# Optimization experiments

Measured on AMD Instinct MI355X. Metric: run time of the kernel, lower is better.

## Reference

```python
import jax, jax.numpy as jnp
import numpy as np

# --- hashgrid config (from __init__: num_levels=16, level_dim=4, base_res=2, log2_hashmap_size=19, desired_res=2048) ---
NUM_LEVELS = 16
LEVEL_DIM = 4
BASE_RES = 2
DESIRED_RES = 2048
TABLE_SIZE = 2 ** 19
_b = np.exp((np.log(DESIRED_RES) - np.log(BASE_RES)) / (NUM_LEVELS - 1))
SCALES = BASE_RES * _b ** np.arange(NUM_LEVELS) - 1.0          # instant-ngp per-level scale
RES = (np.ceil(SCALES) + 1).astype(np.int64)                   # per-level grid resolution
PRIME = np.uint32(2654435761)                                  # 2D spatial hash prime


def softplus10(x):
    return jax.nn.softplus(10.0 * x) / 10.0


def hash_encode(u, tables):
    """u: [P,2] in [0,1]; tables: [L, TABLE_SIZE, LEVEL_DIM]. Returns [P, L*LEVEL_DIM]."""
    outs = []
    for l in range(NUM_LEVELS):
        s = float(SCALES[l])
        res = int(RES[l])
        pos = u * s + 0.5
        pf = jnp.floor(pos)
        fr = pos - pf                      # bilinear fractions, [P,2]
        pi = pf.astype(jnp.int32)
        acc = None
        for dx in (0, 1):
            for dy in (0, 1):
                cx = pi[:, 0] + dx
                cy = pi[:, 1] + dy
                if res * res <= TABLE_SIZE:
                    idx = cy * res + cx                                   # dense level
                else:
                    idx = (cx.astype(jnp.uint32) ^ (cy.astype(jnp.uint32) * PRIME)) % jnp.uint32(TABLE_SIZE)
                    idx = idx.astype(jnp.int32)                           # hashed level
                wx = fr[:, 0] if dx else 1.0 - fr[:, 0]
                wy = fr[:, 1] if dy else 1.0 - fr[:, 1]
                term = tables[l][idx] * (wx * wy)[:, None]                # gather + bilerp
                acc = term if acc is None else acc + term
        outs.append(acc)
    return jnp.concatenate(outs, axis=-1)


def setup_inputs() -> dict:
    key = jax.random.key(0)
    ks = jax.random.split(key, 4)
    B, N, T = 4, 2048, 192
    x = jax.random.normal(ks[0], (B, N, T, 2), jnp.float32)
    embeddings = jax.random.normal(ks[1], (NUM_LEVELS, TABLE_SIZE, LEVEL_DIM), jnp.float32) * 1e-2
    W0 = jax.random.normal(ks[2], (64, 64), jnp.float32) / 8.0
    b0 = jnp.zeros((64,), jnp.float32)
    W1 = jax.random.normal(ks[3], (64, 1), jnp.float32) / 8.0
    b1 = jnp.zeros((1,), jnp.float32)
    return {"x": x, "embeddings": embeddings, "W0": W0, "b0": b0, "W1": W1, "b1": b1}


def reference(x, embeddings, W0, b0, W1, b1):
    B, N, T = x.shape[:3]
    xf = x.reshape(-1, T, 2)                       # [B*N, T, 2]
    rays_o = xf[:, 0]
    rd = xf[:, -1] - xf[:, 0]
    rd = rd / jnp.linalg.norm(rd, axis=-1, keepdims=True)
    z = jnp.linspace(0.0, 2.0, T)                  # [T]
    sample_dist = 1.0 / T
    xys = rays_o[:, None, :] + rd[:, None, :] * z[None, :, None]   # [B*N, T, 2]
    xys = jnp.clip(xys, -1.0, 1.0)                 # aabb clamp [-1,-1,1,1]
    u = (xys.reshape(-1, 2) + 1.0) * 0.5           # map [-bound,bound] -> [0,1], bound=1
    feats = hash_encode(u, embeddings)             # [P, 64]
    h = softplus10(feats @ W0 + b0)
    sigma = softplus10(h @ W1 + b1).reshape(-1, T) # [B*N, T]
    deltas = jnp.concatenate([jnp.full((1,), sample_dist, sigma.dtype), z[1:] - z[:-1]])  # [T]
    density = (deltas[None, :] * sigma).reshape(B, N, T)
    return density
```

## Files before the change

### kernel.cpp

```cpp
#include <hip/hip_runtime.h>
#include <cmath>
#include <algorithm>

#define NUM_LEVELS 16
#define TABLE_SIZE 524288
#define TMASK (TABLE_SIZE - 1)
#define HASH_PRIME 2654435761u
#define T_SAMPLES 192
#define BLOCK 256
#define PTS 64
#define CHUNK 4096

typedef __bf16 bf16x8 __attribute__((ext_vector_type(8)));
typedef __bf16 bf16x4 __attribute__((ext_vector_type(4)));
typedef float f32x4 __attribute__((ext_vector_type(4)));
typedef short s16x4 __attribute__((ext_vector_type(4)));

struct LvlParams {
    float s[NUM_LEVELS];
    int   res[NUM_LEVELS];
    int   hashed[NUM_LEVELS];
    int   off[NUM_LEVELS];
    int   used[NUM_LEVELS];
};

__device__ __forceinline__ float softplus10(float x) {
    float t = 10.0f * x;
    float e = __expf(-fabsf(t));
    return (fmaxf(t, 0.0f) + __logf(1.0f + e)) * 0.1f;
}

__device__ __forceinline__ void corner_idx(int cx, int cy, int res, int hashed,
                                           int& i00, int& i01, int& i10, int& i11) {
    if (hashed) {
        unsigned hy0 = (unsigned)cy * HASH_PRIME;
        unsigned hy1 = (unsigned)(cy + 1) * HASH_PRIME;
        i00 = (int)(((unsigned)cx ^ hy0) & TMASK);
        i01 = (int)(((unsigned)cx ^ hy1) & TMASK);
        i10 = (int)(((unsigned)(cx + 1) ^ hy0) & TMASK);
        i11 = (int)(((unsigned)(cx + 1) ^ hy1) & TMASK);
    } else {
        i00 = cy * res + cx; i10 = i00 + 1;
        i01 = i00 + res;     i11 = i01 + 1;
    }
}

__device__ __forceinline__ bf16x4 lerp4(f32x4 c00, f32x4 c01, f32x4 c10, f32x4 c11,
                                        float fx, float fy) {
    float w00 = (1.0f - fx) * (1.0f - fy), w01 = (1.0f - fx) * fy;
    float w10 = fx * (1.0f - fy),          w11 = fx * fy;
    f32x4 a = c00 * w00 + c01 * w01 + c10 * w10 + c11 * w11;
    bf16x4 r;
    r[0] = (__bf16)a.x; r[1] = (__bf16)a.y; r[2] = (__bf16)a.z; r[3] = (__bf16)a.w;
    return r;
}

__global__ void prep(const float* __restrict__ W0, __bf16* __restrict__ w0f,
                     float* __restrict__ sArr, int* __restrict__ resArr,
                     int* __restrict__ hashArr, int* __restrict__ offArr,
                     int* __restrict__ usedArr, LvlParams lp) {
    const int t = threadIdx.x;
    if (t < NUM_LEVELS) {
        sArr[t] = lp.s[t]; resArr[t] = lp.res[t]; hashArr[t] = lp.hashed[t];
        offArr[t] = lp.off[t]; usedArr[t] = lp.used[t];
    }
    #pragma unroll
    for (int i = 0; i < 16; ++i) {
        int f = t * 16 + i;
        int j = f & 7, lx = (f >> 3) & 15, q = (f >> 7) & 3, nt = (f >> 9) & 3, kc = f >> 11;
        int k = kc * 32 + q * 8 + j;
        int n = nt * 16 + lx;
        w0f[f] = (__bf16)W0[k * 64 + n];
    }
}

__global__ void prep_tables(const float* __restrict__ emb, short* __restrict__ embq,
                            float* __restrict__ scaleArr,
                            const int* __restrict__ offArr, const int* __restrict__ usedArr) {
    __shared__ float red[256];
    const int l    = blockIdx.y;
    const int used = usedArr[l];
    const int base = blockIdx.x * CHUNK;
    if (base >= used) return;
    const int t = threadIdx.x;
    const float* src = emb + ((size_t)l * TABLE_SIZE + base) * 4;

    f32x4 v[16];
    float m = 0.0f;
    #pragma unroll
    for (int i = 0; i < 16; ++i) {
        int e = t + 256 * i;
        if (base + e < used) {
            v[i] = *(const f32x4*)(src + (size_t)e * 4);
            m = fmaxf(m, fmaxf(fmaxf(fabsf(v[i].x), fabsf(v[i].y)),
                               fmaxf(fabsf(v[i].z), fabsf(v[i].w))));
        } else v[i] = (f32x4)(0.0f);
    }
    red[t] = m;
    __syncthreads();
    for (int s = 128; s > 0; s >>= 1) {
        if (t < s) red[t] = fmaxf(red[t], red[t + s]);
        __syncthreads();
    }
    const float mx  = red[0];
    const float inv = (mx > 0.0f) ? (32767.0f / mx) : 0.0f;
    const int chunkIdx = (offArr[l] >> 12) + blockIdx.x;
    if (t == 0) scaleArr[chunkIdx] = (mx > 0.0f) ? (mx / 32767.0f) : 0.0f;

    short* dst = embq + (size_t)(offArr[l] + base) * 4;
    #pragma unroll
    for (int i = 0; i < 16; ++i) {
        int e = t + 256 * i;
        if (base + e < used) {
            s16x4 q;
            q[0] = (short)__float2int_rn(v[i].x * inv);
            q[1] = (short)__float2int_rn(v[i].y * inv);
            q[2] = (short)__float2int_rn(v[i].z * inv);
            q[3] = (short)__float2int_rn(v[i].w * inv);
            *(s16x4*)(dst + (size_t)e * 4) = q;
        }
    }
}

template<bool QT>
__launch_bounds__(BLOCK, 8)
__global__ void nerf_fused(const float* __restrict__ x,
                           const float* __restrict__ emb,
                           const short* __restrict__ embq,
                           const float* __restrict__ scaleArr,
                           const __bf16* __restrict__ w0f,
                           const float* __restrict__ sArr,
                           const int* __restrict__ resArr,
                           const int* __restrict__ hashArr,
                           const int* __restrict__ offArr,
                           const float* __restrict__ b0,
                           const float* __restrict__ W1,
                           const float* __restrict__ b1,
                           float* __restrict__ out) {
    __shared__ __align__(16) __bf16 feT[NUM_LEVELS * PTS * 4];

    const int tid  = threadIdx.x;
    const int lane = tid & 63, w = tid >> 6;

    const int gp  = blockIdx.x * PTS + lane;
    const int ray = gp / T_SAMPLES;
    const int t   = gp - ray * T_SAMPLES;

    const float2 o  = *(const float2*)(x + (size_t)ray * (T_SAMPLES * 2));
    const float2 ep = *(const float2*)(x + (size_t)ray * (T_SAMPLES * 2) + (T_SAMPLES - 1) * 2);
    float rdx = ep.x - o.x, rdy = ep.y - o.y;
    float inv = 1.0f / sqrtf(rdx * rdx + rdy * rdy);
    rdx *= inv; rdy *= inv;
    const float z = (float)((double)t * (2.0 / 191.0));
    float px = fminf(fmaxf(o.x + rdx * z, -1.0f), 1.0f);
    float py = fminf(fmaxf(o.y + rdy * z, -1.0f), 1.0f);
    const float ux = (px + 1.0f) * 0.5f;
    const float uy = (py + 1.0f) * 0.5f;

    const int l3 = w + 12;

    f32x4 c3v[4]; float fx3, fy3;
    {
        float s = sArr[l3];
        float posx = ux * s + 0.5f, posy = uy * s + 0.5f;
        float pfx = floorf(posx), pfy = floorf(posy);
        fx3 = posx - pfx; fy3 = posy - pfy;
        int cx = (int)pfx, cy = (int)pfy;
        int i00, i01, i10, i11;
        corner_idx(cx, cy, resArr[l3], hashArr[l3], i00, i01, i10, i11);
        if (QT) {
            const s16x4* tb = (const s16x4*)embq + offArr[l3];
            const int cb = offArr[l3] >> 12;
            s16x4 r0 = tb[i00], r1 = tb[i01], r2 = tb[i10], r3 = tb[i11];
            c3v[0] = __builtin_convertvector(r0, f32x4) * scaleArr[cb + (i00 >> 12)];
            c3v[1] = __builtin_convertvector(r1, f32x4) * scaleArr[cb + (i01 >> 12)];
            c3v[2] = __builtin_convertvector(r2, f32x4) * scaleArr[cb + (i10 >> 12)];
            c3v[3] = __builtin_convertvector(r3, f32x4) * scaleArr[cb + (i11 >> 12)];
        } else {
            const f32x4* tb = (const f32x4*)(emb + (size_t)l3 * (TABLE_SIZE * 4));
            c3v[0] = tb[i00]; c3v[1] = tb[i01]; c3v[2] = tb[i10]; c3v[3] = tb[i11];
        }
    }

    #pragma unroll
    for (int li = 0; li < 3; ++li) {
        const int l = w + li * 4;
        float s = sArr[l];
        float posx = ux * s + 0.5f, posy = uy * s + 0.5f;
        float pfx = floorf(posx), pfy = floorf(posy);
        float fx = posx - pfx, fy = posy - pfy;
        int cx = (int)pfx, cy = (int)pfy;
        int res = resArr[l];
        int i00 = cy * res + cx, i10 = i00 + 1, i01 = i00 + res, i11 = i01 + 1;
        f32x4 a, b, c, d;
        if (QT) {
            const s16x4* tb = (const s16x4*)embq + offArr[l];
            const int cb = offArr[l] >> 12;
            s16x4 r0 = tb[i00], r1 = tb[i01], r2 = tb[i10], r3 = tb[i11];
            a = __builtin_convertvector(r0, f32x4) * scaleArr[cb + (i00 >> 12)];
            b = __builtin_convertvector(r1, f32x4) * scaleArr[cb + (i01 >> 12)];
            c = __builtin_convertvector(r2, f32x4) * scaleArr[cb + (i10 >> 12)];
            d = __builtin_convertvector(r3, f32x4) * scaleArr[cb + (i11 >> 12)];
        } else {
            const f32x4* tb = (const f32x4*)(emb + (size_t)l * (TABLE_SIZE * 4));
            a = tb[i00]; b = tb[i01]; c = tb[i10]; d = tb[i11];
        }
        *(bf16x4*)&feT[(l * PTS + lane) * 4] = lerp4(a, b, c, d, fx, fy);
    }

    *(bf16x4*)&feT[(l3 * PTS + lane) * 4] = lerp4(c3v[0], c3v[1], c3v[2], c3v[3], fx3, fy3);

    __syncthreads();

    const int lx = lane & 15, q = lane >> 4;
    const int p  = w * 16 + lx;

    f32x4 acc[4];
    #pragma unroll
    for (int nt = 0; nt < 4; ++nt) acc[nt] = (f32x4)(0.0f);

    #pragma unroll
    for (int kc = 0; kc < 2; ++kc) {
        const int la = kc * 8 + 2 * q;
        bf16x4 lo = *(const bf16x4*)&feT[(la * PTS + p) * 4];
        bf16x4 hi = *(const bf16x4*)&feT[((la + 1) * PTS + p) * 4];
        bf16x8 afr = __builtin_shufflevector(lo, hi, 0, 1, 2, 3, 4, 5, 6, 7);
        #pragma unroll
        for (int nt = 0; nt < 4; ++nt) {
            bf16x8 bfr = *(const bf16x8*)(w0f + (size_t)(((kc * 4 + nt) * 4 + q) * 16 + lx) * 8);
            acc[nt] = __builtin_amdgcn_mfma_f32_16x16x32_bf16(afr, bfr, acc[nt], 0, 0, 0);
        }
    }

    float b0v[4], w1v[4];
    #pragma unroll
    for (int nt = 0; nt < 4; ++nt) {
        b0v[nt] = b0[nt * 16 + lx];
        w1v[nt] = W1[nt * 16 + lx];
    }
    const float b1v = b1[0];
    const float d0 = (float)(1.0 / 192.0);
    const float d1 = (float)(2.0 / 191.0);

    float part[4];
    #pragma unroll
    for (int r = 0; r < 4; ++r) {
        float pp = 0.0f;
        #pragma unroll
        for (int nt = 0; nt < 4; ++nt)
            pp += softplus10(acc[nt][r] + b0v[nt]) * w1v[nt];
        pp += __shfl_xor(pp, 1, 64);
        pp += __shfl_xor(pp, 2, 64);
        pp += __shfl_xor(pp, 4, 64);
        pp += __shfl_xor(pp, 8, 64);
        part[r] = pp;
    }
    if (lx == 0) {
        const int g0 = blockIdx.x * PTS + w * 16 + q * 4;
        const int tt = g0 % T_SAMPLES;
        f32x4 ov;
        ov.x = softplus10(part[0] + b1v) * (tt == 0 ? d0 : d1);
        ov.y = softplus10(part[1] + b1v) * d1;
        ov.z = softplus10(part[2] + b1v) * d1;
        ov.w = softplus10(part[3] + b1v) * d1;
        *(f32x4*)(out + g0) = ov;
    }
}

extern "C" void kernel_launch(void* const* d_in, const int* in_sizes, int n_in,
                              void* d_out, int out_size, void* d_ws, size_t ws_size,
                              hipStream_t stream) {
    const float* x   = (const float*)d_in[0];
    const float* emb = (const float*)d_in[1];
    const float* W0  = (const float*)d_in[2];
    const float* b0  = (const float*)d_in[3];
    const float* W1  = (const float*)d_in[4];
    const float* b1  = (const float*)d_in[5];
    float* out = (float*)d_out;

    char* ws = (char*)d_ws;
    __bf16* w0f    = (__bf16*)ws;
    float*  sArr   = (float*)(ws + 8192);
    int*    resArr = (int*)(ws + 8256);
    int*    hashArr= (int*)(ws + 8320);
    int*    offArr = (int*)(ws + 8384);
    int*    usedArr= (int*)(ws + 8448);
    float*  scaleArr = (float*)(ws + 8704);
    short*  embq   = (short*)(ws + 16384);

    LvlParams lp;
    const double bb = std::exp((std::log(2048.0) - std::log(2.0)) / 15.0);
    int off = 0, maxUsed = 0;
    for (int l = 0; l < NUM_LEVELS; ++l) {
        double sc = 2.0 * std::pow(bb, (double)l) - 1.0;
        int rr = (int)std::ceil(sc) + 1;
        lp.s[l] = (float)sc;
        lp.res[l] = rr;
        lp.hashed[l] = ((long long)rr * (long long)rr > (long long)TABLE_SIZE) ? 1 : 0;
        int used;
        if (lp.hashed[l]) {
            used = TABLE_SIZE;
        } else {
            long long cmax = (long long)std::floor(sc + 0.5) + 1;
            long long u = cmax * (long long)rr + cmax + 1 + (rr + 2);
            used = (int)std::min((long long)TABLE_SIZE, u);
        }
        lp.off[l]  = off;
        lp.used[l] = used;
        off += (used + CHUNK - 1) & ~(CHUNK - 1);
        if (used > maxUsed) maxUsed = used;
    }
    const size_t need = 16384 + (size_t)off * 4 * sizeof(short);
    const bool useQ = ws_size >= need;

    prep<<<1, 256, 0, stream>>>(W0, w0f, sArr, resArr, hashArr, offArr, usedArr, lp);

    const int nblk = out_size / PTS;
    if (useQ) {
        dim3 pg((maxUsed + CHUNK - 1) / CHUNK, NUM_LEVELS);
        prep_tables<<<pg, 256, 0, stream>>>(emb, embq, scaleArr, offArr, usedArr);
        nerf_fused<true><<<nblk, BLOCK, 0, stream>>>(x, emb, embq, scaleArr, w0f,
                                                     sArr, resArr, hashArr, offArr,
                                                     b0, W1, b1, out);
    } else {
        nerf_fused<false><<<nblk, BLOCK, 0, stream>>>(x, emb, embq, scaleArr, w0f,
                                                      sArr, resArr, hashArr, offArr,
                                                      b0, W1, b1, out);
    }
}
```

Measured before the change: 356.1 us.

## Store hash tables in fp16, drop per-chunk scales, and switch MFMA to f16

Replaces the int16 per-chunk-scaled table quantization with a plain fp16 table copy, which removes the max-reduction in the prep kernel and the scale lookups on every gather. Bilinear interpolation now runs in packed fp16, and the MLP's first layer uses the f16 MFMA instead of bf16. The softplus constants are folded into the bias and W1 scaling, and the hash recomputes hy1 by adding the prime instead of multiplying. fp16 has less dynamic range than the scaled int16 format, and doing the interpolation in half precision adds rounding error.

```diff
diff --git a/kernel.cpp b/kernel.cpp
--- a/kernel.cpp
+++ b/kernel.cpp
@@ -11,10 +11,11 @@
 #define PTS 64
 #define CHUNK 4096
 
-typedef __bf16 bf16x8 __attribute__((ext_vector_type(8)));
-typedef __bf16 bf16x4 __attribute__((ext_vector_type(4)));
+typedef _Float16 f16;
+typedef f16 f16x2 __attribute__((ext_vector_type(2)));
+typedef f16 f16x4 __attribute__((ext_vector_type(4)));
+typedef f16 f16x8 __attribute__((ext_vector_type(8)));
 typedef float f32x4 __attribute__((ext_vector_type(4)));
-typedef short s16x4 __attribute__((ext_vector_type(4)));
 
 struct LvlParams {
     float s[NUM_LEVELS];
@@ -34,7 +35,7 @@
                                            int& i00, int& i01, int& i10, int& i11) {
     if (hashed) {
         unsigned hy0 = (unsigned)cy * HASH_PRIME;
-        unsigned hy1 = (unsigned)(cy + 1) * HASH_PRIME;
+        unsigned hy1 = hy0 + HASH_PRIME;
         i00 = (int)(((unsigned)cx ^ hy0) & TMASK);
         i01 = (int)(((unsigned)cx ^ hy1) & TMASK);
         i10 = (int)(((unsigned)(cx + 1) ^ hy0) & TMASK);
@@ -45,17 +46,25 @@
     }
 }
 
-__device__ __forceinline__ bf16x4 lerp4(f32x4 c00, f32x4 c01, f32x4 c10, f32x4 c11,
+__device__ __forceinline__ f16x4 lerp4h(f16x4 c00, f16x4 c01, f16x4 c10, f16x4 c11,
+                                        float fx, float fy) {
+    float gx = 1.0f - fx, gy = 1.0f - fy;
+    f16 w00 = (f16)(gx * gy), w01 = (f16)(gx * fy);
+    f16 w10 = (f16)(fx * gy), w11 = (f16)(fx * fy);
+    f16x4 v00 = {w00, w00, w00, w00}, v01 = {w01, w01, w01, w01};
+    f16x4 v10 = {w10, w10, w10, w10}, v11 = {w11, w11, w11, w11};
+    return c00 * v00 + c01 * v01 + c10 * v10 + c11 * v11;
+}
+
+__device__ __forceinline__ f16x4 lerp4f(f32x4 c00, f32x4 c01, f32x4 c10, f32x4 c11,
                                         float fx, float fy) {
     float w00 = (1.0f - fx) * (1.0f - fy), w01 = (1.0f - fx) * fy;
     float w10 = fx * (1.0f - fy),          w11 = fx * fy;
     f32x4 a = c00 * w00 + c01 * w01 + c10 * w10 + c11 * w11;
-    bf16x4 r;
-    r[0] = (__bf16)a.x; r[1] = (__bf16)a.y; r[2] = (__bf16)a.z; r[3] = (__bf16)a.w;
-    return r;
-}
-
-__global__ void prep(const float* __restrict__ W0, __bf16* __restrict__ w0f,
+    return __builtin_convertvector(a, f16x4);
+}
+
+__global__ void prep(const float* __restrict__ W0, f16* __restrict__ w0f,
                      float* __restrict__ sArr, int* __restrict__ resArr,
                      int* __restrict__ hashArr, int* __restrict__ offArr,
                      int* __restrict__ usedArr, LvlParams lp) {
@@ -70,54 +79,25 @@
         int j = f & 7, lx = (f >> 3) & 15, q = (f >> 7) & 3, nt = (f >> 9) & 3, kc = f >> 11;
         int k = kc * 32 + q * 8 + j;
         int n = nt * 16 + lx;
-        w0f[f] = (__bf16)W0[k * 64 + n];
-    }
-}
-
-__global__ void prep_tables(const float* __restrict__ emb, short* __restrict__ embq,
-                            float* __restrict__ scaleArr,
+        w0f[f] = (f16)W0[k * 64 + n];
+    }
+}
+
+__global__ void prep_tables(const float* __restrict__ emb, f16* __restrict__ embq,
                             const int* __restrict__ offArr, const int* __restrict__ usedArr) {
-    __shared__ float red[256];
     const int l    = blockIdx.y;
     const int used = usedArr[l];
     const int base = blockIdx.x * CHUNK;
     if (base >= used) return;
     const int t = threadIdx.x;
     const float* src = emb + ((size_t)l * TABLE_SIZE + base) * 4;
-
-    f32x4 v[16];
-    float m = 0.0f;
+    f16* dst = embq + (size_t)(offArr[l] + base) * 4;
     #pragma unroll
     for (int i = 0; i < 16; ++i) {
         int e = t + 256 * i;
         if (base + e < used) {
-            v[i] = *(const f32x4*)(src + (size_t)e * 4);
-            m = fmaxf(m, fmaxf(fmaxf(fabsf(v[i].x), fabsf(v[i].y)),
-                               fmaxf(fabsf(v[i].z), fabsf(v[i].w))));
-        } else v[i] = (f32x4)(0.0f);
-    }
-    red[t] = m;
-    __syncthreads();
-    for (int s = 128; s > 0; s >>= 1) {
-        if (t < s) red[t] = fmaxf(red[t], red[t + s]);
-        __syncthreads();
-    }
-    const float mx  = red[0];
-    const float inv = (mx > 0.0f) ? (32767.0f / mx) : 0.0f;
-    const int chunkIdx = (offArr[l] >> 12) + blockIdx.x;
-    if (t == 0) scaleArr[chunkIdx] = (mx > 0.0f) ? (mx / 32767.0f) : 0.0f;
-
-    short* dst = embq + (size_t)(offArr[l] + base) * 4;
-    #pragma unroll
-    for (int i = 0; i < 16; ++i) {
-        int e = t + 256 * i;
-        if (base + e < used) {
-            s16x4 q;
-            q[0] = (short)__float2int_rn(v[i].x * inv);
-            q[1] = (short)__float2int_rn(v[i].y * inv);
-            q[2] = (short)__float2int_rn(v[i].z * inv);
-            q[3] = (short)__float2int_rn(v[i].w * inv);
-            *(s16x4*)(dst + (size_t)e * 4) = q;
+            f32x4 v = *(const f32x4*)(src + (size_t)e * 4);
+            *(f16x4*)(dst + (size_t)e * 4) = __builtin_convertvector(v, f16x4);
         }
     }
 }
@@ -126,9 +106,8 @@
 __launch_bounds__(BLOCK, 8)
 __global__ void nerf_fused(const float* __restrict__ x,
                            const float* __restrict__ emb,
-                           const short* __restrict__ embq,
-                           const float* __restrict__ scaleArr,
-                           const __bf16* __restrict__ w0f,
+                           const f16* __restrict__ embq,
+                           const f16* __restrict__ w0f,
                            const float* __restrict__ sArr,
                            const int* __restrict__ resArr,
                            const int* __restrict__ hashArr,
@@ -137,7 +116,7 @@
                            const float* __restrict__ W1,
                            const float* __restrict__ b1,
                            float* __restrict__ out) {
-    __shared__ __align__(16) __bf16 feT[NUM_LEVELS * PTS * 4];
+    __shared__ __align__(16) f16 feT[NUM_LEVELS * PTS * 4];
 
     const int tid  = threadIdx.x;
     const int lane = tid & 63, w = tid >> 6;
@@ -159,7 +138,7 @@
 
     const int l3 = w + 12;
 
-    f32x4 c3v[4]; float fx3, fy3;
+    f16x4 c3v[4]; float fx3, fy3;
     {
         float s = sArr[l3];
         float posx = ux * s + 0.5f, posy = uy * s + 0.5f;
@@ -169,16 +148,15 @@
         int i00, i01, i10, i11;
         corner_idx(cx, cy, resArr[l3], hashArr[l3], i00, i01, i10, i11);
         if (QT) {
-            const s16x4* tb = (const s16x4*)embq + offArr[l3];
-            const int cb = offArr[l3] >> 12;
-            s16x4 r0 = tb[i00], r1 = tb[i01], r2 = tb[i10], r3 = tb[i11];
-            c3v[0] = __builtin_convertvector(r0, f32x4) * scaleArr[cb + (i00 >> 12)];
-            c3v[1] = __builtin_convertvector(r1, f32x4) * scaleArr[cb + (i01 >> 12)];
-            c3v[2] = __builtin_convertvector(r2, f32x4) * scaleArr[cb + (i10 >> 12)];
-            c3v[3] = __builtin_convertvector(r3, f32x4) * scaleArr[cb + (i11 >> 12)];
+            const f16x4* tb = (const f16x4*)embq + offArr[l3];
+            c3v[0] = tb[i00]; c3v[1] = tb[i01]; c3v[2] = tb[i10]; c3v[3] = tb[i11];
         } else {
             const f32x4* tb = (const f32x4*)(emb + (size_t)l3 * (TABLE_SIZE * 4));
-            c3v[0] = tb[i00]; c3v[1] = tb[i01]; c3v[2] = tb[i10]; c3v[3] = tb[i11];
+            f32x4 a = tb[i00], b = tb[i01], c = tb[i10], d = tb[i11];
+            c3v[0] = __builtin_convertvector(a, f16x4);
+            c3v[1] = __builtin_convertvector(b, f16x4);
+            c3v[2] = __builtin_convertvector(c, f16x4);
+            c3v[3] = __builtin_convertvector(d, f16x4);
         }
     }
 
@@ -192,23 +170,18 @@
         int cx = (int)pfx, cy = (int)pfy;
         int res = resArr[l];
         int i00 = cy * res + cx, i10 = i00 + 1, i01 = i00 + res, i11 = i01 + 1;
-        f32x4 a, b, c, d;
         if (QT) {
-            const s16x4* tb = (const s16x4*)embq + offArr[l];
-            const int cb = offArr[l] >> 12;
-            s16x4 r0 = tb[i00], r1 = tb[i01], r2 = tb[i10], r3 = tb[i11];
-            a = __builtin_convertvector(r0, f32x4) * scaleArr[cb + (i00 >> 12)];
-            b = __builtin_convertvector(r1, f32x4) * scaleArr[cb + (i01 >> 12)];
-            c = __builtin_convertvector(r2, f32x4) * scaleArr[cb + (i10 >> 12)];
-            d = __builtin_convertvector(r3, f32x4) * scaleArr[cb + (i11 >> 12)];
+            const f16x4* tb = (const f16x4*)embq + offArr[l];
+            f16x4 a = tb[i00], b = tb[i01], c = tb[i10], d = tb[i11];
+            *(f16x4*)&feT[(l * PTS + lane) * 4] = lerp4h(a, b, c, d, fx, fy);
         } else {
             const f32x4* tb = (const f32x4*)(emb + (size_t)l * (TABLE_SIZE * 4));
-            a = tb[i00]; b = tb[i01]; c = tb[i10]; d = tb[i11];
-        }
-        *(bf16x4*)&feT[(l * PTS + lane) * 4] = lerp4(a, b, c, d, fx, fy);
-    }
-
-    *(bf16x4*)&feT[(l3 * PTS + lane) * 4] = lerp4(c3v[0], c3v[1], c3v[2], c3v[3], fx3, fy3);
+            f32x4 a = tb[i00], b = tb[i01], c = tb[i10], d = tb[i11];
+            *(f16x4*)&feT[(l * PTS + lane) * 4] = lerp4f(a, b, c, d, fx, fy);
+        }
+    }
+
+    *(f16x4*)&feT[(l3 * PTS + lane) * 4] = lerp4h(c3v[0], c3v[1], c3v[2], c3v[3], fx3, fy3);
 
     __syncthreads();
 
@@ -222,21 +195,21 @@
     #pragma unroll
     for (int kc = 0; kc < 2; ++kc) {
         const int la = kc * 8 + 2 * q;
-        bf16x4 lo = *(const bf16x4*)&feT[(la * PTS + p) * 4];
-        bf16x4 hi = *(const bf16x4*)&feT[((la + 1) * PTS + p) * 4];
-        bf16x8 afr = __builtin_shufflevector(lo, hi, 0, 1, 2, 3, 4, 5, 6, 7);
+        f16x4 lo = *(const f16x4*)&feT[(la * PTS + p) * 4];
+        f16x4 hi = *(const f16x4*)&feT[((la + 1) * PTS + p) * 4];
+        f16x8 afr = __builtin_shufflevector(lo, hi, 0, 1, 2, 3, 4, 5, 6, 7);
         #pragma unroll
         for (int nt = 0; nt < 4; ++nt) {
-            bf16x8 bfr = *(const bf16x8*)(w0f + (size_t)(((kc * 4 + nt) * 4 + q) * 16 + lx) * 8);
-            acc[nt] = __builtin_amdgcn_mfma_f32_16x16x32_bf16(afr, bfr, acc[nt], 0, 0, 0);
-        }
-    }
-
-    float b0v[4], w1v[4];
+            f16x8 bfr = *(const f16x8*)(w0f + (size_t)(((kc * 4 + nt) * 4 + q) * 16 + lx) * 8);
+            acc[nt] = __builtin_amdgcn_mfma_f32_16x16x32_f16(afr, bfr, acc[nt], 0, 0, 0);
+        }
+    }
+
+    float b010[4], w1s[4];
     #pragma unroll
     for (int nt = 0; nt < 4; ++nt) {
-        b0v[nt] = b0[nt * 16 + lx];
-        w1v[nt] = W1[nt * 16 + lx];
+        b010[nt] = b0[nt * 16 + lx] * 10.0f;
+        w1s[nt]  = W1[nt * 16 + lx] * 0.1f;
     }
     const float b1v = b1[0];
     const float d0 = (float)(1.0 / 192.0);
@@ -247,8 +220,12 @@
     for (int r = 0; r < 4; ++r) {
         float pp = 0.0f;
         #pragma unroll
-        for (int nt = 0; nt < 4; ++nt)
-            pp += softplus10(acc[nt][r] + b0v[nt]) * w1v[nt];
+        for (int nt = 0; nt < 4; ++nt) {
+            float t10 = fmaf(acc[nt][r], 10.0f, b010[nt]);
+            float e   = __expf(-fabsf(t10));
+            float sp  = fmaxf(t10, 0.0f) + __logf(1.0f + e);
+            pp = fmaf(sp, w1s[nt], pp);
+        }
         pp += __shfl_xor(pp, 1, 64);
         pp += __shfl_xor(pp, 2, 64);
         pp += __shfl_xor(pp, 4, 64);
@@ -279,14 +256,13 @@
     float* out = (float*)d_out;
 
     char* ws = (char*)d_ws;
-    __bf16* w0f    = (__bf16*)ws;
+    f16*    w0f    = (f16*)ws;
     float*  sArr   = (float*)(ws + 8192);
     int*    resArr = (int*)(ws + 8256);
     int*    hashArr= (int*)(ws + 8320);
     int*    offArr = (int*)(ws + 8384);
     int*    usedArr= (int*)(ws + 8448);
-    float*  scaleArr = (float*)(ws + 8704);
-    short*  embq   = (short*)(ws + 16384);
+    f16*    embq   = (f16*)(ws + 16384);
 
     LvlParams lp;
     const double bb = std::exp((std::log(2048.0) - std::log(2.0)) / 15.0);
@@ -310,7 +286,7 @@
         off += (used + CHUNK - 1) & ~(CHUNK - 1);
         if (used > maxUsed) maxUsed = used;
     }
-    const size_t need = 16384 + (size_t)off * 4 * sizeof(short);
+    const size_t need = 16384 + (size_t)off * 4 * sizeof(f16);
     const bool useQ = ws_size >= need;
 
     prep<<<1, 256, 0, stream>>>(W0, w0f, sArr, resArr, hashArr, offArr, usedArr, lp);
@@ -318,12 +294,12 @@
     const int nblk = out_size / PTS;
     if (useQ) {
         dim3 pg((maxUsed + CHUNK - 1) / CHUNK, NUM_LEVELS);
-        prep_tables<<<pg, 256, 0, stream>>>(emb, embq, scaleArr, offArr, usedArr);
-        nerf_fused<true><<<nblk, BLOCK, 0, stream>>>(x, emb, embq, scaleArr, w0f,
+        prep_tables<<<pg, 256, 0, stream>>>(emb, embq, offArr, usedArr);
+        nerf_fused<true><<<nblk, BLOCK, 0, stream>>>(x, emb, embq, w0f,
                                                      sArr, resArr, hashArr, offArr,
                                                      b0, W1, b1, out);
     } else {
-        nerf_fused<false><<<nblk, BLOCK, 0, stream>>>(x, emb, embq, scaleArr, w0f,
+        nerf_fused<false><<<nblk, BLOCK, 0, stream>>>(x, emb, embq, w0f,
                                                       sArr, resArr, hashArr, offArr,
                                                       b0, W1, b1, out);
     }
```

Result: faster. 342.9 us (-3.7%).
